# Kernel tuning notes

Measured on AMD Instinct MI355X. Metric: run time of the kernel, lower is better.

Reference implementation:

```python
import math
import jax, jax.numpy as jnp
import numpy as np

E = 1024          # n_embd
H = 16            # n_head
KVH = 8           # n_kv_head
N_REP = H // KVH  # 2
HD = E // H // 2  # 32, differential attention halves head_dim
DEPTH = 12
LAMBDA_INIT = 0.8 - 0.6 * math.exp(-0.3 * DEPTH)
EPS = 1e-6
ROPE_BASE = 10000.0


def rope_tables(T):
    inv_freq = 1.0 / (ROPE_BASE ** (np.arange(0, HD, 2, dtype=np.float32) / HD))
    t = np.arange(T, dtype=np.float32)
    freqs = np.outer(t, inv_freq)  # [T, HD/2]
    return jnp.asarray(np.cos(freqs)), jnp.asarray(np.sin(freqs))


def apply_rope(x, cos, sin):
    # x: [B, T, nH, HD]; cos/sin: [T, HD/2] broadcast to [1,T,1,HD/2]
    d = x.shape[-1] // 2
    c = cos[None, :, None, :]
    s = sin[None, :, None, :]
    x1, x2 = x[..., :d], x[..., d:]
    return jnp.concatenate([x1 * c + x2 * s, -x1 * s + x2 * c], axis=-1)


def causal_attn(q, k, v, scale):
    # q: [B,T,H,HD], k: [B,T,H,HD], v: [B,T,H,Dv] -> [B,T,H,Dv]
    T = q.shape[1]
    mask = jnp.tril(jnp.ones((T, T), dtype=bool))
    s = jnp.einsum('bthd,bshd->bhts', q, k) * scale
    s = jnp.where(mask[None, None], s, jnp.finfo(s.dtype).min)
    p = jax.nn.softmax(s, axis=-1)
    return jnp.einsum('bhts,bshd->bthd', p, v)


def setup_inputs() -> dict:
    key = jax.random.key(0)
    ks = jax.random.split(key, 10)
    s = 0.02
    return {
        'x': jax.random.normal(ks[0], (4, 1024, E), jnp.float32),
        'Wq': jax.random.normal(ks[1], (E, E), jnp.float32) * s,
        'Wk': jax.random.normal(ks[2], (E, E // N_REP), jnp.float32) * s,
        'Wv': jax.random.normal(ks[3], (E, E // N_REP), jnp.float32) * s,
        'Wo': jax.random.normal(ks[4], (E, E), jnp.float32) * s,
        'lambda_q1': jax.random.normal(ks[5], (HD,), jnp.float32) * 0.1,
        'lambda_k1': jax.random.normal(ks[6], (HD,), jnp.float32) * 0.1,
        'lambda_q2': jax.random.normal(ks[7], (HD,), jnp.float32) * 0.1,
        'lambda_k2': jax.random.normal(ks[8], (HD,), jnp.float32) * 0.1,
        'rms_w': jnp.ones((2 * HD,), jnp.float32),
    }


def reference(x, Wq, Wk, Wv, Wo, lambda_q1, lambda_k1, lambda_q2, lambda_k2, rms_w):
    B, T, _ = x.shape
    q = (x @ Wq).reshape(B, T, 2 * H, HD)
    k = (x @ Wk).reshape(B, T, 2 * KVH, HD)
    v = (x @ Wv).reshape(B, T, KVH, 2, HD)

    cos, sin = rope_tables(T)
    q = apply_rope(q, cos, sin)
    k = apply_rope(k, cos, sin)

    q = q.reshape(B, T, H, 2, HD)
    k = k.reshape(B, T, KVH, 2, HD)
    q1, q2 = q[:, :, :, 0], q[:, :, :, 1]
    k1, k2 = k[:, :, :, 0], k[:, :, :, 1]
    # concat v1||v2 so each softmax is computed once against 2*HD-wide V
    vcat = v.reshape(B, T, KVH, 2 * HD)

    # GQA: repeat kv heads to match query heads
    k1 = jnp.repeat(k1, N_REP, axis=2)
    k2 = jnp.repeat(k2, N_REP, axis=2)
    vcat = jnp.repeat(vcat, N_REP, axis=2)

    scale = HD ** -0.5  # flash_attn default softmax scale
    attn1 = causal_attn(q1, k1, vcat, scale)  # [B,T,H,2*HD] = cat(attn11, attn12)
    attn2 = causal_attn(q2, k2, vcat, scale)  # [B,T,H,2*HD] = cat(attn21, attn22)

    lambda_1 = jnp.exp(jnp.sum(lambda_q1 * lambda_k1))
    lambda_2 = jnp.exp(jnp.sum(lambda_q2 * lambda_k2))
    lambda_full = lambda_1 - lambda_2 + LAMBDA_INIT

    attn = attn1 - lambda_full * attn2
    # RMSNorm over last dim (2*HD)
    rms = jnp.sqrt(jnp.mean(attn * attn, axis=-1, keepdims=True) + EPS)
    attn = (attn / rms) * rms_w
    attn = attn * (1.0 - LAMBDA_INIT)

    attn = attn.reshape(B, T, H * 2 * HD)
    return attn @ Wo
```

## Files before the change

kernel.cpp:

```cpp
#include <hip/hip_runtime.h>

typedef unsigned short u16;
typedef unsigned int   u32;
typedef __attribute__((ext_vector_type(8))) short short8;
typedef __attribute__((ext_vector_type(4))) float f32x4;
typedef __attribute__((ext_vector_type(16))) float f32x16;
typedef __attribute__((ext_vector_type(4))) u32 u32x4;
typedef __attribute__((ext_vector_type(2))) u32 u32x2;

#define LAMBDA_INIT_F 0.78360576653162444f
#define SCALE_QK      0.17677669529663687f


__device__ __forceinline__ u16 f2bf(float f) {
  u32 u = __float_as_uint(f);
  u32 r = (u + 0x7fffu + ((u >> 16) & 1u)) >> 16;
  return (u16)r;
}
__device__ __forceinline__ float bf2f(u16 h) {
  return __uint_as_float(((u32)h) << 16);
}
__device__ __forceinline__ void gload_lds16(const u16* g, u16* l) {
  __builtin_amdgcn_global_load_lds((const __attribute__((address_space(1))) u32*)g,
                                   (__attribute__((address_space(3))) u32*)l, 16, 0, 0);
}


__global__ void k_cvt_x(const float* __restrict__ x, u16* __restrict__ xb) {
  int id = blockIdx.x * 256 + threadIdx.x;
  float4 v = ((const float4*)x)[id];
  u16* o = xb + (size_t)id * 4;
  o[0] = f2bf(v.x); o[1] = f2bf(v.y); o[2] = f2bf(v.z); o[3] = f2bf(v.w);
}

__global__ void k_transpose(const float* __restrict__ Wq, const float* __restrict__ Wk,
                            const float* __restrict__ Wv, const float* __restrict__ Wo,
                            u16* __restrict__ wt, u16* __restrict__ wot) {
  __shared__ float tile[32][33];
  const float* src; u16* dst; int N;
  switch (blockIdx.z) {
    case 0: src = Wq; dst = wt;               N = 1024; break;
    case 1: src = Wk; dst = wt + 1024 * 1024; N = 512;  break;
    case 2: src = Wv; dst = wt + 1536 * 1024; N = 512;  break;
    default: src = Wo; dst = wot;             N = 1024; break;
  }
  int nb = blockIdx.x * 32, kb = blockIdx.y * 32;
  if (nb >= N) return;
  int tx = threadIdx.x, ty = threadIdx.y;
  #pragma unroll
  for (int i = 0; i < 32; i += 8)
    tile[ty + i][tx] = src[(size_t)(kb + ty + i) * N + nb + tx];
  __syncthreads();
  #pragma unroll
  for (int i = 0; i < 32; i += 8)
    dst[(size_t)(nb + ty + i) * 1024 + kb + tx] = f2bf(tile[tx][ty + i]);
}

__global__ void k_rope_tab(float* __restrict__ cosT, float* __restrict__ sinT) {
  int id = blockIdx.x * 256 + threadIdx.x;
  if (id >= 16384) return;
  int t = id >> 4, i = id & 15;
  float inv = powf(10000.0f, -(float)i * (1.0f / 16.0f));
  float f = (float)t * inv;
  float sv, cv; sincosf(f, &sv, &cv);
  cosT[id] = cv; sinT[id] = sv;
}


template<int OBF16>
__global__ __launch_bounds__(256) void gemm_bt(const u16* __restrict__ A, const u16* __restrict__ Bt,
                                               void* __restrict__ Cv, int M, int N, int K, int ldc) {
  __shared__ u16 As[128 * 32];
  __shared__ u16 Bs[128 * 32];
  const int tid = threadIdx.x;
  const int wid = tid >> 6, lane = tid & 63;
  const int m0 = blockIdx.y * 128, n0 = blockIdx.x * 128;
  const int wr = wid >> 1, wc = wid & 1;
  f32x4 acc[4][4];
  #pragma unroll
  for (int m = 0; m < 4; ++m)
    #pragma unroll
    for (int n = 0; n < 4; ++n) acc[m][n] = (f32x4){0.f, 0.f, 0.f, 0.f};
  const int lrow = lane >> 2;
  const int lcol = (lane & 3) * 8;
  for (int k0 = 0; k0 < K; k0 += 32) {
    #pragma unroll
    for (int i = 0; i < 2; ++i) {
      const int ch = wid + i * 4;
      const int row = ch * 16 + lrow;
      gload_lds16(A  + (size_t)(m0 + row) * K + k0 + lcol, &As[ch * 512]);
      gload_lds16(Bt + (size_t)(n0 + row) * K + k0 + lcol, &Bs[ch * 512]);
    }
    __syncthreads();
    const int fr = lane & 15, fc = (lane >> 4) * 8;
    short8 af[4], bfr[4];
    #pragma unroll
    for (int m = 0; m < 4; ++m) af[m]  = *(const short8*)&As[(wr * 64 + m * 16 + fr) * 32 + fc];
    #pragma unroll
    for (int n = 0; n < 4; ++n) bfr[n] = *(const short8*)&Bs[(wc * 64 + n * 16 + fr) * 32 + fc];
    #pragma unroll
    for (int m = 0; m < 4; ++m)
      #pragma unroll
      for (int n = 0; n < 4; ++n)
        acc[m][n] = __builtin_amdgcn_mfma_f32_16x16x32_bf16(af[m], bfr[n], acc[m][n], 0, 0, 0);
    __syncthreads();
  }
  const int fr = lane & 15, fg = lane >> 4;
  #pragma unroll
  for (int m = 0; m < 4; ++m)
    #pragma unroll
    for (int n = 0; n < 4; ++n)
      #pragma unroll
      for (int r = 0; r < 4; ++r) {
        const int row = m0 + wr * 64 + m * 16 + fg * 4 + r;
        const int col = n0 + wc * 64 + n * 16 + fr;
        if (OBF16) ((u16*)Cv)[(size_t)row * ldc + col] = f2bf(acc[m][n][r]);
        else       ((float*)Cv)[(size_t)row * ldc + col] = acc[m][n][r];
      }
}


__global__ void k_rope_reorg(const u16* __restrict__ qkvb, const float* __restrict__ cosT,
                             const float* __restrict__ sinT,
                             u16* __restrict__ q1, u16* __restrict__ q2,
                             u16* __restrict__ k1, u16* __restrict__ k2) {
  int id = blockIdx.x * 256 + threadIdx.x;
  const int NQ = 4096 * 32 * 16;
  const int NK = 4096 * 16 * 16;
  if (id < NQ) {
    int m = id >> 9, r = id & 511;
    int qh = r >> 4, d = r & 15;
    int b = m >> 10, t = m & 1023;
    float x1 = bf2f(qkvb[(size_t)m * 2048 + qh * 32 + d]);
    float x2 = bf2f(qkvb[(size_t)m * 2048 + qh * 32 + d + 16]);
    float c = cosT[t * 16 + d], s = sinT[t * 16 + d];
    float o1 = (x1 * c + x2 * s) * SCALE_QK, o2 = (x2 * c - x1 * s) * SCALE_QK;
    int h = qh >> 1, comp = qh & 1;
    u16* dst = comp ? q2 : q1;
    size_t base = ((size_t)(b * 16 + h) * 1024 + t) * 32 + d;
    dst[base] = f2bf(o1); dst[base + 16] = f2bf(o2);
  } else if (id < NQ + NK) {
    int id2 = id - NQ;
    int m = id2 >> 8, r = id2 & 255;
    int kh = r >> 4, d = r & 15;
    int b = m >> 10, t = m & 1023;
    float x1 = bf2f(qkvb[(size_t)m * 2048 + 1024 + kh * 32 + d]);
    float x2 = bf2f(qkvb[(size_t)m * 2048 + 1024 + kh * 32 + d + 16]);
    float c = cosT[t * 16 + d], s = sinT[t * 16 + d];
    float o1 = x1 * c + x2 * s, o2 = x2 * c - x1 * s;
    int kvh = kh >> 1, comp = kh & 1;
    u16* dst = comp ? k2 : k1;
    size_t base = ((size_t)(b * 8 + kvh) * 1024 + t) * 32 + d;
    dst[base] = f2bf(o1); dst[base + 16] = f2bf(o2);
  }
}

__global__ void k_vt(const u16* __restrict__ qkvb, u16* __restrict__ vt) {
  __shared__ u16 tile[32][34];
  int bh = blockIdx.z;
  int b = bh >> 3, kvh = bh & 7;
  int t0 = blockIdx.x * 32, j0 = blockIdx.y * 32;
  int tx = threadIdx.x, ty = threadIdx.y;
  const u16* src = qkvb + (size_t)b * 1024 * 2048 + 1536 + kvh * 64;
  #pragma unroll
  for (int i = 0; i < 32; i += 8)
    tile[ty + i][tx] = src[(size_t)(t0 + ty + i) * 2048 + j0 + tx];
  __syncthreads();
  u16* dst = vt + ((size_t)bh * 64 + j0) * 1024 + t0;
  #pragma unroll
  for (int i = 0; i < 32; i += 8)
    dst[(size_t)(ty + i) * 1024 + tx] = tile[tx][ty + i];
}


#define KSTR 40
#define VSTR 88
#define PSTR 88

__global__ __launch_bounds__(256) void attn_mfma(
    const u16* __restrict__ q1g, const u16* __restrict__ q2g,
    const u16* __restrict__ k1g, const u16* __restrict__ k2g,
    const u16* __restrict__ vtg,
    float* __restrict__ a1, float* __restrict__ a2) {
  __shared__ u16 Kl[64 * KSTR];
  __shared__ u16 Vl[64 * VSTR];
  __shared__ u16 Pl[4 * 32 * PSTR];

  const int bid = blockIdx.x;
  const int y = bid & 7, xx = (bid >> 3) & 7, g = bid >> 6;
  const int qb = (xx & 1) ? (xx >> 1) : (7 - (xx >> 1));
  const int prob = g * 8 + y;
  const int comp = prob & 1, h = (prob >> 1) & 15, b = prob >> 5;
  const int tid = threadIdx.x;
  const int w = tid >> 6, lane = tid & 63;
  const int hi = lane >> 5, c = lane & 31;

  const u16* Qc  = (comp ? q2g : q1g) + (size_t)(b * 16 + h) * 1024 * 32;
  const u16* Kc  = (comp ? k2g : k1g) + (size_t)(b * 8 + (h >> 1)) * 1024 * 32;
  const u16* Vtc = vtg + (size_t)(b * 8 + (h >> 1)) * 64 * 1024;

  const int qbase = qb * 128;
  const int q = qbase + w * 32 + c;
  const int qmaxw = qbase + w * 32 + 31;

  short8 qf0 = *(const short8*)&Qc[(size_t)q * 32 + hi * 8];
  short8 qf1 = *(const short8*)&Qc[(size_t)q * 32 + 16 + hi * 8];

  f32x16 acc0, acc1;
  #pragma unroll
  for (int r = 0; r < 16; ++r) { acc0[r] = 0.f; acc1[r] = 0.f; }
  float m_run = -1e30f, l_run = 0.f;

  const int ntiles = qb * 2 + 2;

  const int krow = tid >> 2, kseg = tid & 3;
  const int vrow = tid >> 3, vseg = tid & 7;
  u32x4 kr, vr0, vr1;
  kr  = *(const u32x4*)&Kc[(size_t)krow * 32 + kseg * 8];
  vr0 = *(const u32x4*)&Vtc[(size_t)vrow * 1024 + vseg * 8];
  vr1 = *(const u32x4*)&Vtc[(size_t)(vrow + 32) * 1024 + vseg * 8];

  for (int t = 0; t < ntiles; ++t) {
    const int kv0 = t * 64;
    __syncthreads();
    *(u32x4*)&Kl[krow * KSTR + kseg * 8] = kr;
    *(u32x4*)&Vl[vrow * VSTR + vseg * 8] = vr0;
    *(u32x4*)&Vl[(vrow + 32) * VSTR + vseg * 8] = vr1;
    __syncthreads();
    if (t + 1 < ntiles) {
      const int kn = kv0 + 64;
      kr  = *(const u32x4*)&Kc[(size_t)(kn + krow) * 32 + kseg * 8];
      vr0 = *(const u32x4*)&Vtc[(size_t)vrow * 1024 + kn + vseg * 8];
      vr1 = *(const u32x4*)&Vtc[(size_t)(vrow + 32) * 1024 + kn + vseg * 8];
    }
    if (kv0 > qmaxw) continue;

    f32x16 s0, s1;
    #pragma unroll
    for (int r = 0; r < 16; ++r) { s0[r] = 0.f; s1[r] = 0.f; }
    {
      short8 kf00 = *(const short8*)&Kl[c * KSTR + hi * 8];
      short8 kf01 = *(const short8*)&Kl[c * KSTR + 16 + hi * 8];
      short8 kf10 = *(const short8*)&Kl[(32 + c) * KSTR + hi * 8];
      short8 kf11 = *(const short8*)&Kl[(32 + c) * KSTR + 16 + hi * 8];
      s0 = __builtin_amdgcn_mfma_f32_32x32x16_bf16(kf00, qf0, s0, 0, 0, 0);
      s0 = __builtin_amdgcn_mfma_f32_32x32x16_bf16(kf01, qf1, s0, 0, 0, 0);
      s1 = __builtin_amdgcn_mfma_f32_32x32x16_bf16(kf10, qf0, s1, 0, 0, 0);
      s1 = __builtin_amdgcn_mfma_f32_32x32x16_bf16(kf11, qf1, s1, 0, 0, 0);
    }

    float sv[32];
    #pragma unroll
    for (int r = 0; r < 16; ++r) { sv[r] = s0[r]; sv[16 + r] = s1[r]; }

    if (kv0 + 63 > qbase + w * 32) {
      #pragma unroll
      for (int r = 0; r < 32; ++r) {
        int kv = kv0 + (r >> 4) * 32 + (r & 3) + 8 * ((r >> 2) & 3) + 4 * hi;
        if (kv > q) sv[r] = -1e30f;
      }
    }

    float mt = sv[0];
    #pragma unroll
    for (int r = 1; r < 32; ++r) mt = fmaxf(mt, sv[r]);
    mt = fmaxf(mt, __shfl_xor(mt, 32));
    float m_new = fmaxf(m_run, mt);
    float alpha = __expf(m_run - m_new);
    float tsum = 0.f;
    #pragma unroll
    for (int r = 0; r < 32; ++r) { sv[r] = __expf(sv[r] - m_new); tsum += sv[r]; }
    tsum += __shfl_xor(tsum, 32);
    l_run = l_run * alpha + tsum;
    m_run = m_new;
    #pragma unroll
    for (int r = 0; r < 16; ++r) { acc0[r] *= alpha; acc1[r] *= alpha; }

    u16* Pw = &Pl[(w * 32 + c) * PSTR];
    #pragma unroll
    for (int half = 0; half < 2; ++half)
      #pragma unroll
      for (int rr = 0; rr < 4; ++rr) {
        u32 u0 = __float_as_uint(sv[half * 16 + rr * 4 + 0]) + 0x8000u;
        u32 u1 = __float_as_uint(sv[half * 16 + rr * 4 + 1]) + 0x8000u;
        u32 u2 = __float_as_uint(sv[half * 16 + rr * 4 + 2]) + 0x8000u;
        u32 u3 = __float_as_uint(sv[half * 16 + rr * 4 + 3]) + 0x8000u;
        u32x2 wv;
        wv[0] = (u0 >> 16) | (u1 & 0xffff0000u);
        wv[1] = (u2 >> 16) | (u3 & 0xffff0000u);
        *(u32x2*)&Pw[half * 32 + rr * 8 + hi * 4] = wv;
      }

    const u16* Pr = &Pl[(w * 32 + c) * PSTR];
    #pragma unroll
    for (int kc = 0; kc < 4; ++kc) {
      short8 pf  = *(const short8*)&Pr[kc * 16 + hi * 8];
      short8 vf0 = *(const short8*)&Vl[c * VSTR + kc * 16 + hi * 8];
      short8 vf1 = *(const short8*)&Vl[(32 + c) * VSTR + kc * 16 + hi * 8];
      acc0 = __builtin_amdgcn_mfma_f32_32x32x16_bf16(vf0, pf, acc0, 0, 0, 0);
      acc1 = __builtin_amdgcn_mfma_f32_32x32x16_bf16(vf1, pf, acc1, 0, 0, 0);
    }
  }

  float inv = 1.f / l_run;
  float* ao = (comp ? a2 : a1) + ((size_t)(b * 1024 + q)) * 1024 + h * 64;
  #pragma unroll
  for (int rr = 0; rr < 4; ++rr) {
    float4 o0 = { acc0[rr * 4 + 0] * inv, acc0[rr * 4 + 1] * inv,
                  acc0[rr * 4 + 2] * inv, acc0[rr * 4 + 3] * inv };
    float4 o1 = { acc1[rr * 4 + 0] * inv, acc1[rr * 4 + 1] * inv,
                  acc1[rr * 4 + 2] * inv, acc1[rr * 4 + 3] * inv };
    *(float4*)&ao[rr * 8 + hi * 4] = o0;
    *(float4*)&ao[32 + rr * 8 + hi * 4] = o1;
  }
}


__global__ void k_diff_rms(const float* __restrict__ a1, const float* __restrict__ a2in,
                           const float* __restrict__ lq1, const float* __restrict__ lk1,
                           const float* __restrict__ lq2, const float* __restrict__ lk2,
                           const float* __restrict__ rmsw, u16* __restrict__ out) {
  int id = blockIdx.x * 256 + threadIdx.x;
  if (id >= 65536) return;
  float s1 = 0.f, s2 = 0.f;
  #pragma unroll
  for (int i = 0; i < 32; ++i) { s1 += lq1[i] * lk1[i]; s2 += lq2[i] * lk2[i]; }
  float lam = __expf(s1) - __expf(s2) + LAMBDA_INIT_F;
  const float* p1 = a1 + (size_t)id * 64;
  const float* p2 = a2in + (size_t)id * 64;
  float y[64]; float ss = 0.f;
  #pragma unroll
  for (int d = 0; d < 64; ++d) { float v = p1[d] - lam * p2[d]; y[d] = v; ss += v * v; }
  float inv = rsqrtf(ss * (1.f / 64.f) + 1e-6f) * (1.f - LAMBDA_INIT_F);
  u16* o = out + (size_t)id * 64;
  #pragma unroll
  for (int d = 0; d < 64; ++d) o[d] = f2bf(y[d] * inv * rmsw[d]);
}


extern "C" void kernel_launch(void* const* d_in, const int* in_sizes, int n_in,
                              void* d_out, int out_size, void* d_ws, size_t ws_size,
                              hipStream_t stream) {
  (void)in_sizes; (void)n_in; (void)out_size; (void)ws_size;
  const float* x    = (const float*)d_in[0];
  const float* Wq   = (const float*)d_in[1];
  const float* Wk   = (const float*)d_in[2];
  const float* Wv   = (const float*)d_in[3];
  const float* Wo   = (const float*)d_in[4];
  const float* lq1  = (const float*)d_in[5];
  const float* lk1  = (const float*)d_in[6];
  const float* lq2  = (const float*)d_in[7];
  const float* lk2  = (const float*)d_in[8];
  const float* rmsw = (const float*)d_in[9];
  float* out = (float*)d_out;

  char* ws = (char*)d_ws;
  size_t off = 0;
  auto alloc = [&](size_t bytes) { void* p = ws + off; off += (bytes + 255) & ~(size_t)255; return p; };
  u16*   xb    = (u16*)  alloc(4096ULL * 1024 * 2);
  u16*   wt    = (u16*)  alloc(2048ULL * 1024 * 2);
  u16*   wot   = (u16*)  alloc(1024ULL * 1024 * 2);
  u16*   qkvb  = (u16*)  alloc(4096ULL * 2048 * 2);
  float* cosT  = (float*)alloc(16384ULL * 4);
  float* sinT  = (float*)alloc(16384ULL * 4);
  u16*   q1    = (u16*)  alloc(4ULL * 16 * 1024 * 32 * 2);
  u16*   q2    = (u16*)  alloc(4ULL * 16 * 1024 * 32 * 2);
  u16*   k1    = (u16*)  alloc(4ULL * 8 * 1024 * 32 * 2);
  u16*   k2    = (u16*)  alloc(4ULL * 8 * 1024 * 32 * 2);
  u16*   vt    = (u16*)  alloc(4ULL * 8 * 64 * 1024 * 2);
  float* a1    = (float*)alloc(4096ULL * 1024 * 4);
  float* a2    = (float*)alloc(4096ULL * 1024 * 4);
  u16*   am    = (u16*)  alloc(4096ULL * 1024 * 2);

  hipLaunchKernelGGL(k_cvt_x, dim3(4096), dim3(256), 0, stream, x, xb);
  hipLaunchKernelGGL(k_transpose, dim3(32, 32, 4), dim3(32, 8), 0, stream, Wq, Wk, Wv, Wo, wt, wot);
  hipLaunchKernelGGL(k_rope_tab, dim3(64), dim3(256), 0, stream, cosT, sinT);
  hipLaunchKernelGGL((gemm_bt<1>), dim3(16, 32), dim3(256), 0, stream, xb, wt, (void*)qkvb, 4096, 2048, 1024, 2048);
  hipLaunchKernelGGL(k_rope_reorg, dim3(12288), dim3(256), 0, stream, qkvb, cosT, sinT, q1, q2, k1, k2);
  hipLaunchKernelGGL(k_vt, dim3(32, 2, 32), dim3(32, 8), 0, stream, qkvb, vt);
  hipLaunchKernelGGL(attn_mfma, dim3(1024), dim3(256), 0, stream, q1, q2, k1, k2, vt, a1, a2);
  hipLaunchKernelGGL(k_diff_rms, dim3(256), dim3(256), 0, stream, a1, a2, lq1, lk1, lq2, lk2, rmsw, am);
  hipLaunchKernelGGL((gemm_bt<0>), dim3(8, 32), dim3(256), 0, stream, am, wot, (void*)out, 4096, 1024, 1024, 1024);
}
```

Before: 228.5 us.

## Store attention outputs as bf16 and reorder block-to-query-tile mapping

The attention kernel now writes its two per-component outputs in bf16 instead of fp32, and the diff/RMSNorm kernel reads them with 16-byte vector loads. This halves the intermediate write and read traffic between the two kernels. The block index mapping is also changed so that consecutive blocks pair complementary causal query tiles, aiming for better load balance. The cost is extra rounding of attn1/attn2 before the subtraction, which can amplify error when the two nearly cancel.

```diff
diff --git a/kernel.cpp b/kernel.cpp
--- a/kernel.cpp
+++ b/kernel.cpp
@@ -181,15 +181,16 @@
     const u16* __restrict__ q1g, const u16* __restrict__ q2g,
     const u16* __restrict__ k1g, const u16* __restrict__ k2g,
     const u16* __restrict__ vtg,
-    float* __restrict__ a1, float* __restrict__ a2) {
+    u16* __restrict__ a1, u16* __restrict__ a2) {
   __shared__ u16 Kl[64 * KSTR];
   __shared__ u16 Vl[64 * VSTR];
   __shared__ u16 Pl[4 * 32 * PSTR];
 
   const int bid = blockIdx.x;
-  const int y = bid & 7, xx = (bid >> 3) & 7, g = bid >> 6;
-  const int qb = (xx & 1) ? (xx >> 1) : (7 - (xx >> 1));
-  const int prob = g * 8 + y;
+  const int j = bid & 255, k = bid >> 8;
+  const int prob = j >> 1;
+  const int qtab[2][4] = {{0, 7, 2, 5}, {6, 1, 4, 3}};
+  const int qb = qtab[j & 1][k];
   const int comp = prob & 1, h = (prob >> 1) & 15, b = prob >> 5;
   const int tid = threadIdx.x;
   const int w = tid >> 6, lane = tid & 63;
@@ -303,20 +304,21 @@
   }
 
   float inv = 1.f / l_run;
-  float* ao = (comp ? a2 : a1) + ((size_t)(b * 1024 + q)) * 1024 + h * 64;
+  u16* ao = (comp ? a2 : a1) + ((size_t)(b * 1024 + q)) * 1024 + h * 64;
   #pragma unroll
   for (int rr = 0; rr < 4; ++rr) {
-    float4 o0 = { acc0[rr * 4 + 0] * inv, acc0[rr * 4 + 1] * inv,
-                  acc0[rr * 4 + 2] * inv, acc0[rr * 4 + 3] * inv };
-    float4 o1 = { acc1[rr * 4 + 0] * inv, acc1[rr * 4 + 1] * inv,
-                  acc1[rr * 4 + 2] * inv, acc1[rr * 4 + 3] * inv };
-    *(float4*)&ao[rr * 8 + hi * 4] = o0;
-    *(float4*)&ao[32 + rr * 8 + hi * 4] = o1;
-  }
-}
-
-
-__global__ void k_diff_rms(const float* __restrict__ a1, const float* __restrict__ a2in,
+    u32x2 w0, w1;
+    w0[0] = (u32)f2bf(acc0[rr * 4 + 0] * inv) | ((u32)f2bf(acc0[rr * 4 + 1] * inv) << 16);
+    w0[1] = (u32)f2bf(acc0[rr * 4 + 2] * inv) | ((u32)f2bf(acc0[rr * 4 + 3] * inv) << 16);
+    w1[0] = (u32)f2bf(acc1[rr * 4 + 0] * inv) | ((u32)f2bf(acc1[rr * 4 + 1] * inv) << 16);
+    w1[1] = (u32)f2bf(acc1[rr * 4 + 2] * inv) | ((u32)f2bf(acc1[rr * 4 + 3] * inv) << 16);
+    *(u32x2*)&ao[rr * 8 + hi * 4] = w0;
+    *(u32x2*)&ao[32 + rr * 8 + hi * 4] = w1;
+  }
+}
+
+
+__global__ void k_diff_rms(const u16* __restrict__ a1, const u16* __restrict__ a2in,
                            const float* __restrict__ lq1, const float* __restrict__ lk1,
                            const float* __restrict__ lq2, const float* __restrict__ lk2,
                            const float* __restrict__ rmsw, u16* __restrict__ out) {
@@ -326,15 +328,23 @@
   #pragma unroll
   for (int i = 0; i < 32; ++i) { s1 += lq1[i] * lk1[i]; s2 += lq2[i] * lk2[i]; }
   float lam = __expf(s1) - __expf(s2) + LAMBDA_INIT_F;
-  const float* p1 = a1 + (size_t)id * 64;
-  const float* p2 = a2in + (size_t)id * 64;
-  float y[64]; float ss = 0.f;
-  #pragma unroll
-  for (int d = 0; d < 64; ++d) { float v = p1[d] - lam * p2[d]; y[d] = v; ss += v * v; }
+  const u16* p1 = a1 + (size_t)id * 64;
+  const u16* p2 = a2in + (size_t)id * 64;
+  float yv[64]; float ss = 0.f;
+  #pragma unroll
+  for (int d8 = 0; d8 < 8; ++d8) {
+    short8 v1 = *(const short8*)&p1[d8 * 8];
+    short8 v2 = *(const short8*)&p2[d8 * 8];
+    #pragma unroll
+    for (int jj = 0; jj < 8; ++jj) {
+      float v = bf2f((u16)v1[jj]) - lam * bf2f((u16)v2[jj]);
+      yv[d8 * 8 + jj] = v; ss += v * v;
+    }
+  }
   float inv = rsqrtf(ss * (1.f / 64.f) + 1e-6f) * (1.f - LAMBDA_INIT_F);
   u16* o = out + (size_t)id * 64;
   #pragma unroll
-  for (int d = 0; d < 64; ++d) o[d] = f2bf(y[d] * inv * rmsw[d]);
+  for (int d = 0; d < 64; ++d) o[d] = f2bf(yv[d] * inv * rmsw[d]);
 }
 
 
@@ -368,8 +378,8 @@
   u16*   k1    = (u16*)  alloc(4ULL * 8 * 1024 * 32 * 2);
   u16*   k2    = (u16*)  alloc(4ULL * 8 * 1024 * 32 * 2);
   u16*   vt    = (u16*)  alloc(4ULL * 8 * 64 * 1024 * 2);
-  float* a1    = (float*)alloc(4096ULL * 1024 * 4);
-  float* a2    = (float*)alloc(4096ULL * 1024 * 4);
+  u16*   a1    = (u16*)  alloc(4096ULL * 1024 * 2);
+  u16*   a2    = (u16*)  alloc(4096ULL * 1024 * 2);
   u16*   am    = (u16*)  alloc(4096ULL * 1024 * 2);
 
   hipLaunchKernelGGL(k_cvt_x, dim3(4096), dim3(256), 0, stream, x, xb);
```

Result: faster. 201.9 us (-11.7%).
